# Kernel tuning notes

Measured on AMD Instinct MI355X. Metric: run time of the kernel, lower is better.

Reference implementation:

```python
import jax, jax.numpy as jnp
import numpy as np

N_NODES = 100000
N_EDGES = 1600000
N_GRAPHS = 1000
HID = 64
NEG_SLOPE = 0.2


def _glorot(key, shape):
    fan_in, fan_out = shape[0], shape[-1]
    lim = float(np.sqrt(6.0 / (fan_in + fan_out)))
    return jax.random.uniform(key, shape, jnp.float32, -lim, lim)


def setup_inputs() -> dict:
    key = jax.random.key(0)
    ks = jax.random.split(key, 20)
    x = jax.random.normal(ks[0], (N_NODES, 1), jnp.float32)
    edge_index = jax.random.randint(ks[1], (2, N_EDGES), 0, N_NODES, jnp.int64)
    batch = jnp.sort(jax.random.randint(ks[2], (N_NODES,), 0, N_GRAPHS, jnp.int64))
    inp = {"x": x, "edge_index": edge_index, "batch": batch}
    # GATv2Conv layer 1 (in=3 -> out=HID, 1 head)
    inp["Wl1"] = _glorot(ks[3], (3, HID)); inp["bl1"] = jnp.zeros((HID,), jnp.float32)
    inp["Wr1"] = _glorot(ks[4], (3, HID)); inp["br1"] = jnp.zeros((HID,), jnp.float32)
    inp["a1"] = _glorot(ks[5], (HID, 1))[:, 0]; inp["b1"] = jnp.zeros((HID,), jnp.float32)
    # GATv2Conv layer 2 (HID -> HID)
    inp["Wl2"] = _glorot(ks[6], (HID, HID)); inp["bl2"] = jnp.zeros((HID,), jnp.float32)
    inp["Wr2"] = _glorot(ks[7], (HID, HID)); inp["br2"] = jnp.zeros((HID,), jnp.float32)
    inp["a2"] = _glorot(ks[8], (HID, 1))[:, 0]; inp["b2"] = jnp.zeros((HID,), jnp.float32)
    # lin2 (HID -> 2)
    inp["W3"] = _glorot(ks[9], (HID, 2)); inp["b3"] = jnp.zeros((2,), jnp.float32)
    return inp


def gatv2_layer(x, src, dst, Wl, bl, Wr, br, a, b):
    """GATv2Conv, 1 head, add_self_loops=True, negative_slope=0.2."""
    n = x.shape[0]
    xl = x @ Wl + bl  # source-side transform [N, C]
    xr = x @ Wr + br  # target-side transform [N, C]
    loops = jnp.arange(n, dtype=src.dtype)
    s = jnp.concatenate([src, loops])
    d = jnp.concatenate([dst, loops])
    # per-edge attention logit: a^T LeakyReLU(xl[j] + xr[i])
    e = jax.nn.leaky_relu(xl[s] + xr[d], NEG_SLOPE) @ a  # [E+N]
    # segment softmax over incoming edges of each dst node
    m = jax.ops.segment_max(e, d, num_segments=n)
    ex = jnp.exp(e - m[d])
    denom = jax.ops.segment_sum(ex, d, num_segments=n)
    alpha = ex / denom[d]
    out = jax.ops.segment_sum(alpha[:, None] * xl[s], d, num_segments=n)
    return out + b


def reference(x, edge_index, batch, Wl1, bl1, Wr1, br1, a1, b1,
              Wl2, bl2, Wr2, br2, a2, b2, W3, b3):
    n = x.shape[0]
    src, dst = edge_index[0], edge_index[1]
    ones = jnp.ones((src.shape[0],), jnp.float32)
    deg_in = jax.ops.segment_sum(ones, dst, num_segments=n)   # bincount(dst)
    deg_out = jax.ops.segment_sum(ones, src, num_segments=n)  # bincount(src)
    h = jnp.concatenate([x, deg_in[:, None], deg_out[:, None]], axis=1)  # [N,3]
    h = gatv2_layer(h, src, dst, Wl1, bl1, Wr1, br1, a1, b1)
    h = jnp.tanh(h)
    h = gatv2_layer(h, src, dst, Wl2, bl2, Wr2, br2, a2, b2)
    # global_max_pool over graphs
    g = jax.ops.segment_max(h, batch, num_segments=N_GRAPHS)  # [G, HID]
    return g @ W3 + b3  # [G, 2]
```

## Files before the change

### kernel.cpp

```cpp
#include <hip/hip_runtime.h>
#include <hip/hip_bf16.h>
#include <hip/hip_fp16.h>

#define HID 64
#define NEG_SLOPE 0.2f
#define BLK_E 8192
#define EDGE_CAP 6144
#define NDB 16

typedef _Float16 f16x2 __attribute__((ext_vector_type(2)));


__global__ void k_hist2(const int* __restrict__ src, const int* __restrict__ dst,
                        int* __restrict__ histS, int* __restrict__ histD,
                        int E, int NB, int NBLK) {
    __shared__ int hs[512], hd[512];
    int t = threadIdx.x, blk = blockIdx.x;
    for (int b = t; b < NB; b += 1024) { hs[b] = 0; hd[b] = 0; }
    __syncthreads();
    int base = blk * BLK_E;
    #pragma unroll
    for (int k = 0; k < BLK_E / 1024; ++k) {
        int i = base + k * 1024 + t;
        if (i < E) {
            atomicAdd(&hs[src[i] >> 8], 1);
            atomicAdd(&hd[dst[i] >> 8], 1);
        }
    }
    __syncthreads();
    for (int b = t; b < NB; b += 1024) {
        histS[b * NBLK + blk] = hs[b];
        histD[b * NBLK + blk] = hd[b];
    }
}

__global__ void k_binscan(int* __restrict__ histS, int* __restrict__ histD,
                          int* __restrict__ totS, int* __restrict__ totD,
                          int NB, int NBLK) {
    __shared__ int s[256];
    int b = blockIdx.x;
    int* hist = histS; int* tot = totS;
    if (b >= NB) { b -= NB; hist = histD; tot = totD; }
    int t = threadIdx.x;
    int v = (t < NBLK) ? hist[b * NBLK + t] : 0;
    s[t] = v;
    __syncthreads();
    for (int o = 1; o < 256; o <<= 1) {
        int u = (t >= o) ? s[t - o] : 0;
        __syncthreads();
        s[t] += u;
        __syncthreads();
    }
    if (t < NBLK) hist[b * NBLK + t] = s[t] - v;
    if (t == 255) tot[b] = s[255];
}

__global__ void k_binoffset(const int* __restrict__ totS, const int* __restrict__ totD,
                            int* __restrict__ bsS, int* __restrict__ bsD,
                            int NB, int E, int* __restrict__ row_off, int N) {
    __shared__ int s[512];
    int t = threadIdx.x;
    int v = (t < NB) ? totS[t] : 0;
    s[t] = v; __syncthreads();
    for (int o = 1; o < 512; o <<= 1) {
        int u = (t >= o) ? s[t - o] : 0;
        __syncthreads(); s[t] += u; __syncthreads();
    }
    if (t < NB) bsS[t] = s[t] - v;
    if (t == 0) bsS[NB] = E;
    __syncthreads();
    v = (t < NB) ? totD[t] : 0;
    s[t] = v; __syncthreads();
    for (int o = 1; o < 512; o <<= 1) {
        int u = (t >= o) ? s[t - o] : 0;
        __syncthreads(); s[t] += u; __syncthreads();
    }
    if (t < NB) bsD[t] = s[t] - v;
    if (t == 0) { bsD[NB] = E; row_off[N] = E; }
}

__global__ void k_scatter_bins(const int* __restrict__ src, const int* __restrict__ dst,
                               const int* __restrict__ histS, const int* __restrict__ histD,
                               const int* __restrict__ bsS, const int* __restrict__ bsD,
                               unsigned* __restrict__ packS, unsigned* __restrict__ packD,
                               int E, int NB, int NBLK) {
    __shared__ int baseS[512], baseD[512];
    int t = threadIdx.x, blk = blockIdx.x;
    for (int b = t; b < NB; b += 1024) {
        baseS[b] = bsS[b] + histS[b * NBLK + blk];
        baseD[b] = bsD[b] + histD[b * NBLK + blk];
    }
    __syncthreads();
    int base = blk * BLK_E;
    #pragma unroll
    for (int k = 0; k < BLK_E / 1024; ++k) {
        int i = base + k * 1024 + t;
        if (i < E) {
            int sv = src[i], dv = dst[i];
            int pD = atomicAdd(&baseD[dv >> 8], 1);
            packD[pD] = ((unsigned)(dv & 255) << 24) | (unsigned)sv;
            int pS = atomicAdd(&baseS[sv >> 8], 1);
            packS[pS] = (unsigned)(sv & 255);
        }
    }
}

__global__ void k_csr_bin(const unsigned* __restrict__ packD, const int* __restrict__ bsD,
                          int* __restrict__ row_off, float* __restrict__ deg_in,
                          int* __restrict__ csr_src, int N) {
    __shared__ int cnt[256], off[256], cur[256];
    __shared__ unsigned eb[EDGE_CAP];
    int b = blockIdx.x, t = threadIdx.x;
    int lo = bsD[b], hi = bsD[b + 1], ne = hi - lo;
    bool fits = (ne <= EDGE_CAP);
    if (t < 256) cnt[t] = 0;
    __syncthreads();
    for (int i = t; i < ne; i += 1024) {
        unsigned v = packD[lo + i];
        if (fits) eb[i] = v;
        atomicAdd(&cnt[v >> 24], 1);
    }
    __syncthreads();
    if (t < 256) off[t] = cnt[t];
    __syncthreads();
    for (int o = 1; o < 256; o <<= 1) {
        int u = 0;
        if (t < 256 && t >= o) u = off[t - o];
        __syncthreads();
        if (t < 256) off[t] += u;
        __syncthreads();
    }
    if (t < 256) {
        int ex = off[t] - cnt[t];
        cur[t] = lo + ex;
        int node = b * 256 + t;
        if (node < N) {
            row_off[node] = lo + ex;
            deg_in[node] = (float)cnt[t];
        }
    }
    __syncthreads();
    for (int i = t; i < ne; i += 1024) {
        unsigned v = fits ? eb[i] : packD[lo + i];
        int pos = atomicAdd(&cur[v >> 24], 1);
        csr_src[pos] = (int)(v & 0xFFFFFFu);
    }
}

__global__ void k_cnt_bin(const unsigned* __restrict__ packS, const int* __restrict__ bsS,
                          float* __restrict__ deg_out, int N) {
    __shared__ int cnt[256];
    int b = blockIdx.x, t = threadIdx.x;
    int lo = bsS[b], hi = bsS[b + 1];
    if (t < 256) cnt[t] = 0;
    __syncthreads();
    for (int i = lo + t; i < hi; i += 1024) atomicAdd(&cnt[packS[i] & 255], 1);
    __syncthreads();
    if (t < 256) {
        int node = b * 256 + t;
        if (node < N) deg_out[node] = (float)cnt[t];
    }
}


__global__ void k_deghist(const float* __restrict__ deg_in, int* __restrict__ dhist, int N) {
    __shared__ int h[64];
    int t = threadIdx.x, b = blockIdx.x;
    if (t < 64) h[t] = 0;
    __syncthreads();
    int chunk = (N + NDB - 1) / NDB;
    int lo = b * chunk, hi = lo + chunk; if (hi > N) hi = N;
    for (int i = lo + t; i < hi; i += 1024) {
        int dg = (int)deg_in[i]; if (dg > 63) dg = 63;
        atomicAdd(&h[dg], 1);
    }
    __syncthreads();
    if (t < 64) dhist[t * NDB + b] = h[t];
}

__global__ void k_degscan(int* __restrict__ dhist) {
    __shared__ int s[1024];
    int t = threadIdx.x;
    int v = dhist[t];
    s[t] = v; __syncthreads();
    for (int o = 1; o < 1024; o <<= 1) {
        int u = (t >= o) ? s[t - o] : 0;
        __syncthreads(); s[t] += u; __syncthreads();
    }
    dhist[t] = s[t] - v;
}

__global__ void k_degscatter(const float* __restrict__ deg_in, const int* __restrict__ dhist,
                             int* __restrict__ perm, int N) {
    __shared__ int cur[64];
    int t = threadIdx.x, b = blockIdx.x;
    if (t < 64) cur[t] = dhist[t * NDB + b];
    __syncthreads();
    int chunk = (N + NDB - 1) / NDB;
    int lo = b * chunk, hi = lo + chunk; if (hi > N) hi = N;
    for (int i = lo + t; i < hi; i += 1024) {
        int dg = (int)deg_in[i]; if (dg > 63) dg = 63;
        int p = atomicAdd(&cur[dg], 1);
        perm[p] = i;
    }
}


__global__ void k_xfrm1(const float* __restrict__ x, const float* __restrict__ deg_in,
                        const float* __restrict__ deg_out,
                        const float* __restrict__ Wl, const float* __restrict__ bl,
                        const float* __restrict__ Wr, const float* __restrict__ br,
                        __half* __restrict__ A, __half* __restrict__ B, int N) {
    int idx = blockIdx.x * blockDim.x + threadIdx.x;
    if (idx >= N * HID) return;
    int n = idx >> 6, c = idx & 63;
    float h0 = x[n], h1 = deg_in[n], h2 = deg_out[n];
    A[idx] = __float2half(h0 * Wl[c] + h1 * Wl[HID + c] + h2 * Wl[2 * HID + c] + bl[c]);
    B[idx] = __float2half(h0 * Wr[c] + h1 * Wr[HID + c] + h2 * Wr[2 * HID + c] + br[c]);
}

struct H8 { f16x2 h[8]; };

__device__ __forceinline__ f16x2 bch2(unsigned u) {
    return __builtin_bit_cast(f16x2, u);
}

__device__ __forceinline__ H8 ldrow(const uint4* __restrict__ T, size_t base) {
    uint4 r0 = T[base], r1 = T[base + 1];
    H8 o;
    o.h[0] = bch2(r0.x); o.h[1] = bch2(r0.y); o.h[2] = bch2(r0.z); o.h[3] = bch2(r0.w);
    o.h[4] = bch2(r1.x); o.h[5] = bch2(r1.y); o.h[6] = bch2(r1.z); o.h[7] = bch2(r1.w);
    return o;
}

__device__ __forceinline__ float logit16(const H8& a, const H8& x,
                                         const float* __restrict__ awf, f16x2 ns2) {
    float t = 0.0f;
    #pragma unroll
    for (int j = 0; j < 8; ++j) {
        f16x2 s = a.h[j] + x.h[j];
        f16x2 l = __builtin_elementwise_max(s, ns2 * s);
        t = fmaf((float)l.x, awf[2 * j], t);
        t = fmaf((float)l.y, awf[2 * j + 1], t);
    }
    return t;
}

__device__ __forceinline__ void accum16(float* __restrict__ acc, const H8& a, float w) {
    #pragma unroll
    for (int j = 0; j < 8; ++j) {
        acc[2 * j]     = fmaf((float)a.h[j].x, w, acc[2 * j]);
        acc[2 * j + 1] = fmaf((float)a.h[j].y, w, acc[2 * j + 1]);
    }
}

template <bool TANH>
__global__ void k_gat_fused(const int* __restrict__ csr_src, const int* __restrict__ row_off,
                            const int* __restrict__ perm,
                            const __half* __restrict__ Ah, const __half* __restrict__ Bh,
                            const float* __restrict__ aw, const float* __restrict__ bias,
                            float* __restrict__ out, int N) {
    int tid = blockIdx.x * blockDim.x + threadIdx.x;
    int r = tid >> 2;
    int gl = threadIdx.x & 3;
    if (r >= N) return;
    int d = perm[N - 1 - r];

    const uint4* A16 = (const uint4*)Ah;
    const uint4* B16 = (const uint4*)Bh;
    f16x2 ns2;
    ns2.x = (_Float16)NEG_SLOPE; ns2.y = (_Float16)NEG_SLOPE;

    float awf[16];
    {
        const float4* a4 = (const float4*)aw;
        #pragma unroll
        for (int j = 0; j < 4; ++j) {
            float4 v = a4[gl * 4 + j];
            awf[4 * j] = v.x; awf[4 * j + 1] = v.y; awf[4 * j + 2] = v.z; awf[4 * j + 3] = v.w;
        }
    }

    size_t rowbase = (size_t)d * 8 + gl * 2;
    H8 xh = ldrow(B16, rowbase);
    H8 as = ldrow(A16, rowbase);

    float t = logit16(as, xh, awf, ns2);
    t += __shfl_xor(t, 1); t += __shfl_xor(t, 2);
    float m = t, denom = 1.0f;
    float acc[16];
    #pragma unroll
    for (int j = 0; j < 8; ++j) {
        acc[2 * j] = (float)as.h[j].x;
        acc[2 * j + 1] = (float)as.h[j].y;
    }

    int lo = row_off[d], hi = row_off[d + 1];
    int k = lo;
    for (; k + 3 < hi; k += 4) {
        int s0 = csr_src[k], s1 = csr_src[k + 1], s2 = csr_src[k + 2], s3 = csr_src[k + 3];
        H8 a0 = ldrow(A16, (size_t)s0 * 8 + gl * 2);
        H8 a1 = ldrow(A16, (size_t)s1 * 8 + gl * 2);
        H8 a2 = ldrow(A16, (size_t)s2 * 8 + gl * 2);
        H8 a3 = ldrow(A16, (size_t)s3 * 8 + gl * 2);
        float t0 = logit16(a0, xh, awf, ns2);
        float t1 = logit16(a1, xh, awf, ns2);
        float t2 = logit16(a2, xh, awf, ns2);
        float t3 = logit16(a3, xh, awf, ns2);
        t0 += __shfl_xor(t0, 1); t1 += __shfl_xor(t1, 1);
        t2 += __shfl_xor(t2, 1); t3 += __shfl_xor(t3, 1);
        t0 += __shfl_xor(t0, 2); t1 += __shfl_xor(t1, 2);
        t2 += __shfl_xor(t2, 2); t3 += __shfl_xor(t3, 2);
        float mx = fmaxf(fmaxf(t0, t1), fmaxf(t2, t3));
        if (mx > m) {
            float sc = __expf(m - mx);
            denom *= sc;
            #pragma unroll
            for (int j = 0; j < 16; ++j) acc[j] *= sc;
            m = mx;
        }
        float w0 = __expf(t0 - m), w1 = __expf(t1 - m);
        float w2 = __expf(t2 - m), w3 = __expf(t3 - m);
        denom += (w0 + w1) + (w2 + w3);
        accum16(acc, a0, w0);
        accum16(acc, a1, w1);
        accum16(acc, a2, w2);
        accum16(acc, a3, w3);
    }
    for (; k < hi; ++k) {
        int s0 = csr_src[k];
        H8 a0 = ldrow(A16, (size_t)s0 * 8 + gl * 2);
        float t0 = logit16(a0, xh, awf, ns2);
        t0 += __shfl_xor(t0, 1); t0 += __shfl_xor(t0, 2);
        if (t0 > m) {
            float sc = __expf(m - t0);
            denom *= sc;
            #pragma unroll
            for (int j = 0; j < 16; ++j) acc[j] *= sc;
            m = t0;
        }
        float w0 = __expf(t0 - m);
        denom += w0;
        accum16(acc, a0, w0);
    }

    float inv = 1.0f / denom;
    const float4* b4 = (const float4*)bias;
    float4* o4 = (float4*)out;
    #pragma unroll
    for (int j = 0; j < 4; ++j) {
        float4 bv = b4[gl * 4 + j];
        float4 o;
        o.x = acc[4 * j] * inv + bv.x;
        o.y = acc[4 * j + 1] * inv + bv.y;
        o.z = acc[4 * j + 2] * inv + bv.z;
        o.w = acc[4 * j + 3] * inv + bv.w;
        if (TANH) { o.x = tanhf(o.x); o.y = tanhf(o.y); o.z = tanhf(o.z); o.w = tanhf(o.w); }
        o4[(size_t)d * 16 + gl * 4 + j] = o;
    }
}

__global__ __launch_bounds__(512) void k_xfrm2(
        const float* __restrict__ H,
        const float* __restrict__ Wl, const float* __restrict__ bl,
        const float* __restrict__ Wr, const float* __restrict__ br,
        __half* __restrict__ A, __half* __restrict__ B, int N) {
    __shared__ float wls[4096];
    __shared__ float wrs[4096];
    __shared__ float hst[64 * 66];
    int t = threadIdx.x;
    int base = blockIdx.x * 64;

    ((float4*)wls)[t * 2]     = ((const float4*)Wl)[t * 2];
    ((float4*)wls)[t * 2 + 1] = ((const float4*)Wl)[t * 2 + 1];
    ((float4*)wrs)[t * 2]     = ((const float4*)Wr)[t * 2];
    ((float4*)wrs)[t * 2 + 1] = ((const float4*)Wr)[t * 2 + 1];

    #pragma unroll
    for (int u = 0; u < 2; ++u) {
        int j = t * 2 + u;
        int nd = j >> 4, c4 = j & 15;
        int node = base + nd;
        float4 hv = (node < N) ? ((const float4*)H)[(size_t)node * 16 + c4]
                               : make_float4(0.f, 0.f, 0.f, 0.f);
        hst[(c4 * 4 + 0) * 66 + nd] = hv.x;
        hst[(c4 * 4 + 1) * 66 + nd] = hv.y;
        hst[(c4 * 4 + 2) * 66 + nd] = hv.z;
        hst[(c4 * 4 + 3) * 66 + nd] = hv.w;
    }
    __syncthreads();

    int w = t >> 6, l = t & 63;
    float acL[8] = {0, 0, 0, 0, 0, 0, 0, 0};
    float acR[8] = {0, 0, 0, 0, 0, 0, 0, 0};
    #pragma unroll 4
    for (int kk = 0; kk < 64; ++kk) {
        float hv = hst[kk * 66 + l];
        const float4* wl4 = (const float4*)&wls[kk * 64 + w * 8];
        const float4* wr4 = (const float4*)&wrs[kk * 64 + w * 8];
        float4 w0 = wl4[0], w1 = wl4[1];
        float4 r0 = wr4[0], r1 = wr4[1];
        acL[0] = fmaf(hv, w0.x, acL[0]); acL[1] = fmaf(hv, w0.y, acL[1]);
        acL[2] = fmaf(hv, w0.z, acL[2]); acL[3] = fmaf(hv, w0.w, acL[3]);
        acL[4] = fmaf(hv, w1.x, acL[4]); acL[5] = fmaf(hv, w1.y, acL[5]);
        acL[6] = fmaf(hv, w1.z, acL[6]); acL[7] = fmaf(hv, w1.w, acL[7]);
        acR[0] = fmaf(hv, r0.x, acR[0]); acR[1] = fmaf(hv, r0.y, acR[1]);
        acR[2] = fmaf(hv, r0.z, acR[2]); acR[3] = fmaf(hv, r0.w, acR[3]);
        acR[4] = fmaf(hv, r1.x, acR[4]); acR[5] = fmaf(hv, r1.y, acR[5]);
        acR[6] = fmaf(hv, r1.z, acR[6]); acR[7] = fmaf(hv, r1.w, acR[7]);
    }

    int node = base + l;
    if (node < N) {
        float4 bl0 = ((const float4*)bl)[w * 2], bl1 = ((const float4*)bl)[w * 2 + 1];
        float4 br0 = ((const float4*)br)[w * 2], br1 = ((const float4*)br)[w * 2 + 1];
        __half2* A2 = (__half2*)A;
        __half2* B2 = (__half2*)B;
        size_t bo = (size_t)node * 32 + w * 4;
        A2[bo + 0] = __floats2half2_rn(acL[0] + bl0.x, acL[1] + bl0.y);
        A2[bo + 1] = __floats2half2_rn(acL[2] + bl0.z, acL[3] + bl0.w);
        A2[bo + 2] = __floats2half2_rn(acL[4] + bl1.x, acL[5] + bl1.y);
        A2[bo + 3] = __floats2half2_rn(acL[6] + bl1.z, acL[7] + bl1.w);
        B2[bo + 0] = __floats2half2_rn(acR[0] + br0.x, acR[1] + br0.y);
        B2[bo + 1] = __floats2half2_rn(acR[2] + br0.z, acR[3] + br0.w);
        B2[bo + 2] = __floats2half2_rn(acR[4] + br1.x, acR[5] + br1.y);
        B2[bo + 3] = __floats2half2_rn(acR[6] + br1.z, acR[7] + br1.w);
    }
}

__global__ void k_gbounds(const int* __restrict__ batch, int* __restrict__ gstart,
                          int* __restrict__ gend, int N) {
    int i = blockIdx.x * blockDim.x + threadIdx.x;
    if (i >= N) return;
    int g = batch[i];
    if (i == 0 || batch[i - 1] != g) gstart[g] = i;
    if (i == N - 1 || batch[i + 1] != g) gend[g] = i + 1;
}

__global__ void k_pool_seg(const float* __restrict__ C, const float* __restrict__ b2,
                           const int* __restrict__ gstart, const int* __restrict__ gend,
                           float* __restrict__ gout, int G) {
    int w = (int)((blockIdx.x * (size_t)blockDim.x + threadIdx.x) >> 6);
    int lane = threadIdx.x & 63;
    if (w >= G) return;
    float acc = -INFINITY;
    int lo = gstart[w], hi = gend[w];
    for (int i = lo; i < hi; ++i) acc = fmaxf(acc, C[(size_t)i * HID + lane]);
    gout[(size_t)w * HID + lane] = acc + b2[lane];
}

__global__ void k_final(const float* __restrict__ gout, const float* __restrict__ W3,
                        const float* __restrict__ b3, float* __restrict__ out, int G) {
    int idx = blockIdx.x * blockDim.x + threadIdx.x;
    if (idx >= G * 2) return;
    int gi = idx >> 1, j = idx & 1;
    float sum = b3[j];
    #pragma unroll 8
    for (int kk = 0; kk < HID; ++kk) sum += gout[(size_t)gi * HID + kk] * W3[kk * 2 + j];
    out[idx] = sum;
}

extern "C" void kernel_launch(void* const* d_in, const int* in_sizes, int n_in,
                              void* d_out, int out_size, void* d_ws, size_t ws_size,
                              hipStream_t stream) {
    const float* x     = (const float*)d_in[0];
    const int*   ei    = (const int*)d_in[1];
    const int*   batch = (const int*)d_in[2];
    const float* Wl1 = (const float*)d_in[3];
    const float* bl1 = (const float*)d_in[4];
    const float* Wr1 = (const float*)d_in[5];
    const float* br1 = (const float*)d_in[6];
    const float* a1  = (const float*)d_in[7];
    const float* b1  = (const float*)d_in[8];
    const float* Wl2 = (const float*)d_in[9];
    const float* bl2 = (const float*)d_in[10];
    const float* Wr2 = (const float*)d_in[11];
    const float* br2 = (const float*)d_in[12];
    const float* a2  = (const float*)d_in[13];
    const float* b2  = (const float*)d_in[14];
    const float* W3  = (const float*)d_in[15];
    const float* b3  = (const float*)d_in[16];

    const int N = in_sizes[0];
    const int E = in_sizes[1] / 2;
    const int G = out_size / 2;
    const int NB = (N + 255) >> 8;
    const int NBLK = (E + BLK_E - 1) / BLK_E;

    float* ws = (float*)d_ws;
    size_t off = 0;
    float*  C  = ws + off; off += (size_t)N * HID;
    __half* Ah = (__half*)(ws + off); off += (size_t)N * HID / 2;
    __half* Bh = (__half*)(ws + off); off += (size_t)N * HID / 2;
    int*   row_off = (int*)(ws + off); off += N + 1;
    int*   csr_src = (int*)(ws + off); off += E;
    float* deg_in  = ws + off; off += N;
    float* deg_out = ws + off; off += N;
    int*   perm    = (int*)(ws + off); off += N;
    int*   dhist   = (int*)(ws + off); off += 1024;
    int*   bsS  = (int*)(ws + off); off += NB + 1;
    int*   bsD  = (int*)(ws + off); off += NB + 1;
    int*   totS = (int*)(ws + off); off += NB;
    int*   totD = (int*)(ws + off); off += NB;
    int*   gstart = (int*)(ws + off); off += G;
    int*   gend   = (int*)(ws + off); off += G;
    float* gout   = ws + off; off += (size_t)G * HID;

    unsigned* packD = (unsigned*)C;
    unsigned* packS = packD + E;
    int* histS = (int*)(packS + E);
    int* histD = histS + (size_t)NB * NBLK;

    const int* src  = ei;
    const int* dstp = ei + E;

    const int BT = 256;
    dim3 blk(BT);
    int grid_nodeC = (N * HID + BT - 1) / BT;
    int grid_g4    = (int)(((size_t)N * 4 + BT - 1) / BT);
    int grid_x2    = (N + 63) / 64;

    k_hist2<<<NBLK, 1024, 0, stream>>>(src, dstp, histS, histD, E, NB, NBLK);
    k_binscan<<<2 * NB, 256, 0, stream>>>(histS, histD, totS, totD, NB, NBLK);
    k_binoffset<<<1, 512, 0, stream>>>(totS, totD, bsS, bsD, NB, E, row_off, N);
    k_scatter_bins<<<NBLK, 1024, 0, stream>>>(src, dstp, histS, histD, bsS, bsD,
                                              packS, packD, E, NB, NBLK);
    k_csr_bin<<<NB, 1024, 0, stream>>>(packD, bsD, row_off, deg_in, csr_src, N);
    k_cnt_bin<<<NB, 1024, 0, stream>>>(packS, bsS, deg_out, N);

    k_deghist<<<NDB, 1024, 0, stream>>>(deg_in, dhist, N);
    k_degscan<<<1, 1024, 0, stream>>>(dhist);
    k_degscatter<<<NDB, 1024, 0, stream>>>(deg_in, dhist, perm, N);

    (void)hipMemsetAsync(gstart, 0, 2 * (size_t)G * sizeof(int), stream);
    k_gbounds<<<(N + BT - 1) / BT, blk, 0, stream>>>(batch, gstart, gend, N);

    k_xfrm1<<<grid_nodeC, blk, 0, stream>>>(x, deg_in, deg_out, Wl1, bl1, Wr1, br1, Ah, Bh, N);
    k_gat_fused<true><<<grid_g4, blk, 0, stream>>>(csr_src, row_off, perm, Ah, Bh, a1, b1, C, N);

    k_xfrm2<<<grid_x2, 512, 0, stream>>>(C, Wl2, bl2, Wr2, br2, Ah, Bh, N);
    k_gat_fused<false><<<grid_g4, blk, 0, stream>>>(csr_src, row_off, perm, Ah, Bh, a2, b2, C, N);

    k_pool_seg<<<(G * 64 + BT - 1) / BT, blk, 0, stream>>>(C, b2, gstart, gend, gout, G);
    k_final<<<(G * 2 + BT - 1) / BT, blk, 0, stream>>>(gout, W3, b3, (float*)d_out, G);
}
```

Measured before the change: 242.2 us.

## Fuse pooling with final linear, binary-search graph bounds, halve edge block size

Replaces the graph-bounds kernel, memset, pooling and final linear kernels with one kernel. Each wavefront binary-searches the sorted batch array for its graph range, max-pools with 4-way unrolled loads, then does the 64x2 projection via wave shuffles. Separately, the edge histogram block size is halved, which doubles the number of histogram blocks and widens the bin scan to 512 threads for more parallelism in the CSR build. This cuts three launches and a memset, at the cost of redundant binary searches per wave and a larger per-block histogram table.

```diff
diff --git a/kernel.cpp b/kernel.cpp
--- a/kernel.cpp
+++ b/kernel.cpp
@@ -4,7 +4,7 @@
 
 #define HID 64
 #define NEG_SLOPE 0.2f
-#define BLK_E 8192
+#define BLK_E 4096
 #define EDGE_CAP 6144
 #define NDB 16
 
@@ -37,7 +37,7 @@
 __global__ void k_binscan(int* __restrict__ histS, int* __restrict__ histD,
                           int* __restrict__ totS, int* __restrict__ totD,
                           int NB, int NBLK) {
-    __shared__ int s[256];
+    __shared__ int s[512];
     int b = blockIdx.x;
     int* hist = histS; int* tot = totS;
     if (b >= NB) { b -= NB; hist = histD; tot = totD; }
@@ -45,14 +45,14 @@
     int v = (t < NBLK) ? hist[b * NBLK + t] : 0;
     s[t] = v;
     __syncthreads();
-    for (int o = 1; o < 256; o <<= 1) {
+    for (int o = 1; o < 512; o <<= 1) {
         int u = (t >= o) ? s[t - o] : 0;
         __syncthreads();
         s[t] += u;
         __syncthreads();
     }
     if (t < NBLK) hist[b * NBLK + t] = s[t] - v;
-    if (t == 255) tot[b] = s[255];
+    if (t == 511) tot[b] = s[511];
 }
 
 __global__ void k_binoffset(const int* __restrict__ totS, const int* __restrict__ totD,
@@ -428,36 +428,40 @@
     }
 }
 
-__global__ void k_gbounds(const int* __restrict__ batch, int* __restrict__ gstart,
-                          int* __restrict__ gend, int N) {
-    int i = blockIdx.x * blockDim.x + threadIdx.x;
-    if (i >= N) return;
-    int g = batch[i];
-    if (i == 0 || batch[i - 1] != g) gstart[g] = i;
-    if (i == N - 1 || batch[i + 1] != g) gend[g] = i + 1;
-}
-
-__global__ void k_pool_seg(const float* __restrict__ C, const float* __restrict__ b2,
-                           const int* __restrict__ gstart, const int* __restrict__ gend,
-                           float* __restrict__ gout, int G) {
+__global__ void k_pool_final(const float* __restrict__ C, const float* __restrict__ b2,
+                             const int* __restrict__ batch,
+                             const float* __restrict__ W3, const float* __restrict__ b3,
+                             float* __restrict__ out, int N, int G) {
     int w = (int)((blockIdx.x * (size_t)blockDim.x + threadIdx.x) >> 6);
     int lane = threadIdx.x & 63;
     if (w >= G) return;
+    int lo = 0, hi = N;
+    while (lo < hi) { int mid = (lo + hi) >> 1; if (batch[mid] < w) lo = mid + 1; else hi = mid; }
+    int s0 = lo;
+    hi = N;
+    while (lo < hi) { int mid = (lo + hi) >> 1; if (batch[mid] < w + 1) lo = mid + 1; else hi = mid; }
+    int e0 = lo;
+
     float acc = -INFINITY;
-    int lo = gstart[w], hi = gend[w];
-    for (int i = lo; i < hi; ++i) acc = fmaxf(acc, C[(size_t)i * HID + lane]);
-    gout[(size_t)w * HID + lane] = acc + b2[lane];
-}
-
-__global__ void k_final(const float* __restrict__ gout, const float* __restrict__ W3,
-                        const float* __restrict__ b3, float* __restrict__ out, int G) {
-    int idx = blockIdx.x * blockDim.x + threadIdx.x;
-    if (idx >= G * 2) return;
-    int gi = idx >> 1, j = idx & 1;
-    float sum = b3[j];
-    #pragma unroll 8
-    for (int kk = 0; kk < HID; ++kk) sum += gout[(size_t)gi * HID + kk] * W3[kk * 2 + j];
-    out[idx] = sum;
+    int i = s0;
+    for (; i + 3 < e0; i += 4) {
+        float v0 = C[(size_t)i * HID + lane];
+        float v1 = C[(size_t)(i + 1) * HID + lane];
+        float v2 = C[(size_t)(i + 2) * HID + lane];
+        float v3 = C[(size_t)(i + 3) * HID + lane];
+        acc = fmaxf(acc, fmaxf(fmaxf(v0, v1), fmaxf(v2, v3)));
+    }
+    for (; i < e0; ++i) acc = fmaxf(acc, C[(size_t)i * HID + lane]);
+    float v = acc + b2[lane];
+
+    float p0 = v * W3[lane * 2];
+    float p1 = v * W3[lane * 2 + 1];
+    #pragma unroll
+    for (int o = 32; o; o >>= 1) { p0 += __shfl_xor(p0, o); p1 += __shfl_xor(p1, o); }
+    if (lane == 0) {
+        out[(size_t)w * 2]     = p0 + b3[0];
+        out[(size_t)w * 2 + 1] = p1 + b3[1];
+    }
 }
 
 extern "C" void kernel_launch(void* const* d_in, const int* in_sizes, int n_in,
@@ -502,9 +506,6 @@
     int*   bsD  = (int*)(ws + off); off += NB + 1;
     int*   totS = (int*)(ws + off); off += NB;
     int*   totD = (int*)(ws + off); off += NB;
-    int*   gstart = (int*)(ws + off); off += G;
-    int*   gend   = (int*)(ws + off); off += G;
-    float* gout   = ws + off; off += (size_t)G * HID;
 
     unsigned* packD = (unsigned*)C;
     unsigned* packS = packD + E;
@@ -521,7 +522,7 @@
     int grid_x2    = (N + 63) / 64;
 
     k_hist2<<<NBLK, 1024, 0, stream>>>(src, dstp, histS, histD, E, NB, NBLK);
-    k_binscan<<<2 * NB, 256, 0, stream>>>(histS, histD, totS, totD, NB, NBLK);
+    k_binscan<<<2 * NB, 512, 0, stream>>>(histS, histD, totS, totD, NB, NBLK);
     k_binoffset<<<1, 512, 0, stream>>>(totS, totD, bsS, bsD, NB, E, row_off, N);
     k_scatter_bins<<<NBLK, 1024, 0, stream>>>(src, dstp, histS, histD, bsS, bsD,
                                               packS, packD, E, NB, NBLK);
@@ -532,15 +533,12 @@
     k_degscan<<<1, 1024, 0, stream>>>(dhist);
     k_degscatter<<<NDB, 1024, 0, stream>>>(deg_in, dhist, perm, N);
 
-    (void)hipMemsetAsync(gstart, 0, 2 * (size_t)G * sizeof(int), stream);
-    k_gbounds<<<(N + BT - 1) / BT, blk, 0, stream>>>(batch, gstart, gend, N);
-
     k_xfrm1<<<grid_nodeC, blk, 0, stream>>>(x, deg_in, deg_out, Wl1, bl1, Wr1, br1, Ah, Bh, N);
     k_gat_fused<true><<<grid_g4, blk, 0, stream>>>(csr_src, row_off, perm, Ah, Bh, a1, b1, C, N);
 
     k_xfrm2<<<grid_x2, 512, 0, stream>>>(C, Wl2, bl2, Wr2, br2, Ah, Bh, N);
     k_gat_fused<false><<<grid_g4, blk, 0, stream>>>(csr_src, row_off, perm, Ah, Bh, a2, b2, C, N);
 
-    k_pool_seg<<<(G * 64 + BT - 1) / BT, blk, 0, stream>>>(C, b2, gstart, gend, gout, G);
-    k_final<<<(G * 2 + BT - 1) / BT, blk, 0, stream>>>(gout, W3, b3, (float*)d_out, G);
-}
+    k_pool_final<<<(G * 64 + BT - 1) / BT, blk, 0, stream>>>(C, b2, batch, W3, b3,
+                                                             (float*)d_out, N, G);
+}
```

After: 232.6 us. 4.0% less time.
